# Optimization experiments

Hardware: AMD Instinct MI355X
Metric: run time of the kernel (lower is better)

Reference implementation:

```python
import jax, jax.numpy as jnp
import numpy as np

N_QUBITS = 8
N_QLAYERS = 4
N_HEADS = 4
DIM = 2 ** N_QUBITS  # 256


def layer_norm(x, g, b, eps=1e-5):
    m = x.mean(-1, keepdims=True)
    v = ((x - m) ** 2).mean(-1, keepdims=True)
    return (x - m) / jnp.sqrt(v + eps) * g + b


def rx_mat(theta):
    # theta: scalar or [B]; returns [...,2,2] complex64
    h = theta * 0.5
    c = jnp.cos(h).astype(jnp.complex64)
    s = (jnp.sin(h) * (-1j)).astype(jnp.complex64)
    return jnp.stack([jnp.stack([c, s], -1), jnp.stack([s, c], -1)], -2)


def rz_mat(theta):
    h = (theta * 0.5).astype(jnp.complex64)
    e0 = jnp.exp(-1j * h)
    e1 = jnp.exp(1j * h)
    z = jnp.zeros_like(e0)
    return jnp.stack([jnp.stack([e0, z], -1), jnp.stack([z, e1], -1)], -2)


def apply_1q(state, U, wire, n):
    # state: [B, 2**n]; U: [2,2] (shared) or [B,2,2] (per-sample)
    B = state.shape[0]
    left = 2 ** wire
    right = 2 ** (n - 1 - wire)
    s = state.reshape(B, left, 2, right)
    if U.ndim == 2:
        s = jnp.einsum('jk,blkr->bljr', U, s)
    else:
        s = jnp.einsum('bjk,blkr->bljr', U, s)
    return s.reshape(B, 2 ** n)


def apply_cnot(state, ctrl, n):
    # CNOT with control=ctrl, target=ctrl+1 (adjacent wires)
    B = state.shape[0]
    left = 2 ** ctrl
    right = 2 ** (n - 2 - ctrl)
    s = state.reshape(B, left, 4, right)
    s = s[:, :, jnp.array([0, 1, 3, 2]), :]  # swap |10> and |11>
    return s.reshape(B, 2 ** n)


def quantum_expvals(angles, weights):
    # angles: [B, n_qubits] data-encoding angles; weights: [n_layers, 2, n_qubits]
    # Batched statevector sim of: RX(a_i)RZ(a_i) encoding, then per layer
    # RX(w[l,0,i]) RZ(w[l,1,i]) and a CNOT chain; returns <Z_i> per wire.
    n = N_QUBITS
    B = angles.shape[0]
    state = jnp.zeros((B, 2 ** n), jnp.complex64).at[:, 0].set(1.0)
    for i in range(n):
        state = apply_1q(state, rx_mat(angles[:, i]), i, n)
        state = apply_1q(state, rz_mat(angles[:, i]), i, n)
    for l in range(N_QLAYERS):
        for i in range(n):
            state = apply_1q(state, rx_mat(weights[l, 0, i]), i, n)
            state = apply_1q(state, rz_mat(weights[l, 1, i]), i, n)
        for i in range(n - 1):
            state = apply_cnot(state, i, n)
    probs = jnp.abs(state) ** 2  # [B, 2**n] float32
    zs = []
    for i in range(n):
        p = probs.reshape(B, 2 ** i, 2, 2 ** (n - 1 - i)).sum(axis=(1, 3))
        zs.append(p[:, 0] - p[:, 1])
    return jnp.stack(zs, -1)  # [B, n_qubits]


def mha(x, in_w, in_b, out_w, out_b):
    B, S, d = x.shape
    hd = d // N_HEADS
    qkv = x @ in_w.T + in_b  # [B,S,3d]
    q, k, v = jnp.split(qkv, 3, axis=-1)
    sp = lambda t: t.reshape(B, S, N_HEADS, hd).transpose(0, 2, 1, 3)
    q, k, v = sp(q), sp(k), sp(v)
    scores = jnp.einsum('bhqd,bhkd->bhqk', q, k) / np.sqrt(hd).astype(np.float32)
    attn = jax.nn.softmax(scores, axis=-1)
    o = jnp.einsum('bhqk,bhkd->bhqd', attn, v).transpose(0, 2, 1, 3).reshape(B, S, d)
    return o @ out_w.T + out_b


def _forward(x, attn_in_w, attn_in_b, attn_out_w, attn_out_b,
             ln1_g, ln1_b, ln2_g, ln2_b, ln3_g, ln3_b,
             qin_w, qin_b, qweights, qout_w, qout_b,
             ffn_w1, ffn_b1, ffn_w2, ffn_b2):
    attn_out = mha(x, attn_in_w, attn_in_b, attn_out_w, attn_out_b)
    x = layer_norm(x + attn_out, ln1_g, ln1_b)
    x_norm = layer_norm(x, ln3_g, ln3_b)
    B, S, d = x.shape
    flat = x_norm.reshape(B * S, d)
    angles = flat @ qin_w.T + qin_b  # [B*S, n_qubits]
    z = quantum_expvals(angles, qweights)
    q_out = (z @ qout_w.T + qout_b).reshape(B, S, d)
    x = x + q_out
    h = jax.nn.gelu(x @ ffn_w1.T + ffn_b1, approximate=False)  # torch GELU exact
    ffn_out = h @ ffn_w2.T + ffn_b2  # dropout is identity in eval
    return layer_norm(x + ffn_out, ln2_g, ln2_b)


def setup_inputs() -> dict:
    key = jax.random.key(0)
    ks = jax.random.split(key, 10)
    B, S, d, nq, nl = 32, 512, 512, N_QUBITS, N_QLAYERS
    rn = lambda k, sh, sc=0.02: jax.random.normal(k, sh, jnp.float32) * sc
    return {
        'x': jax.random.normal(ks[0], (B, S, d), jnp.float32),
        'attn_in_w': rn(ks[1], (3 * d, d)),
        'attn_in_b': jnp.zeros((3 * d,), jnp.float32),
        'attn_out_w': rn(ks[2], (d, d)),
        'attn_out_b': jnp.zeros((d,), jnp.float32),
        'ln1_g': jnp.ones((d,), jnp.float32), 'ln1_b': jnp.zeros((d,), jnp.float32),
        'ln2_g': jnp.ones((d,), jnp.float32), 'ln2_b': jnp.zeros((d,), jnp.float32),
        'ln3_g': jnp.ones((d,), jnp.float32), 'ln3_b': jnp.zeros((d,), jnp.float32),
        'qin_w': rn(ks[3], (nq, d), 0.05),
        'qin_b': jnp.zeros((nq,), jnp.float32),
        'qweights': jax.random.uniform(ks[4], (nl, 2, nq), jnp.float32, 0.0, 2.0 * np.pi),
        'qout_w': rn(ks[5], (d, nq), 0.1),
        'qout_b': jnp.zeros((d,), jnp.float32),
        'ffn_w1': rn(ks[6], (4 * d, d)),
        'ffn_b1': jnp.zeros((4 * d,), jnp.float32),
        'ffn_w2': rn(ks[7], (d, 4 * d)),
        'ffn_b2': jnp.zeros((d,), jnp.float32),
    }


def reference(x, attn_in_w, attn_in_b, attn_out_w, attn_out_b,
              ln1_g, ln1_b, ln2_g, ln2_b, ln3_g, ln3_b,
              qin_w, qin_b, qweights, qout_w, qout_b,
              ffn_w1, ffn_b1, ffn_w2, ffn_b2):
    return _forward(x, attn_in_w, attn_in_b, attn_out_w, attn_out_b,
                    ln1_g, ln1_b, ln2_g, ln2_b, ln3_g, ln3_b,
                    qin_w, qin_b, qweights, qout_w, qout_b,
                    ffn_w1, ffn_b1, ffn_w2, ffn_b2)
```

## Files before the change

kernel.cpp:

```cpp
#include <hip/hip_runtime.h>
#include <math.h>


typedef __bf16 bf16;
typedef bf16 bf16x8 __attribute__((ext_vector_type(8)));
typedef bf16 bf16x4 __attribute__((ext_vector_type(4)));
typedef float f32x4 __attribute__((ext_vector_type(4)));

__device__ __forceinline__ void gld16(const void* g, void* l) {
  __builtin_amdgcn_global_load_lds(
      (__attribute__((address_space(1))) void*)(void*)g,
      (__attribute__((address_space(3))) void*)l, 16, 0, 0);
}

__device__ __forceinline__ float waveAllSum(float v) {
#pragma unroll
  for (int m = 1; m < 64; m <<= 1) v += __shfl_xor(v, m, 64);
  return v;
}

__device__ __forceinline__ float fast_gelu(float v) {
  float u = 0.79788456080286536f * v * (1.0f + 0.044715f * v * v);
  return v / (1.0f + __expf(-2.0f * u));
}

__global__ __launch_bounds__(256) void cvt_all(
    const float* __restrict__ x, const float* __restrict__ w1,
    const float* __restrict__ w2, const float* __restrict__ w3,
    const float* __restrict__ w4, bf16* __restrict__ xb,
    bf16* __restrict__ b1, bf16* __restrict__ b2, bf16* __restrict__ b3,
    bf16* __restrict__ b4) {
  int i = blockIdx.x * 256 + threadIdx.x;
  const float* src;
  bf16* dst;
  int off;
  if (i < 2097152) {
    src = x; dst = xb; off = i;
  } else if (i < 2097152 + 196608) {
    src = w1; dst = b1; off = i - 2097152;
  } else if (i < 2097152 + 196608 + 65536) {
    src = w2; dst = b2; off = i - (2097152 + 196608);
  } else if (i < 2097152 + 196608 + 65536 + 262144) {
    src = w3; dst = b3; off = i - (2097152 + 196608 + 65536);
  } else {
    src = w4; dst = b4; off = i - (2097152 + 196608 + 65536 + 262144);
  }
  float4 v = ((const float4*)src)[off];
  bf16x4 o = {(bf16)v.x, (bf16)v.y, (bf16)v.z, (bf16)v.w};
  ((bf16x4*)dst)[off] = o;
}

__global__ __launch_bounds__(256) void make_W(const float* __restrict__ qw,
                                              bf16* __restrict__ Wp) {
  __shared__ float gates[32 * 8];
  int tid = threadIdx.x, lane = tid & 63;
  if (tid < 32) {
    int l = tid >> 3, i = tid & 7;
    float ax = qw[l * 16 + i] * 0.5f;
    float az = qw[l * 16 + 8 + i] * 0.5f;
    float cx, sx, cz, sz;
    sincosf(ax, &sx, &cx);
    sincosf(az, &sz, &cz);
    float* g = gates + tid * 8;
    g[0] = cz * cx;   g[1] = -sz * cx;
    g[2] = -sz * sx;  g[3] = -cz * sx;
    g[4] = sz * sx;   g[5] = -cz * sx;
    g[6] = cz * cx;   g[7] = sz * cx;
  }
  __syncthreads();
  int k = blockIdx.x * 4 + (tid >> 6);

  float sr[4], si[4];
#pragma unroll
  for (int l = 0; l < 4; ++l) {
    sr[l] = (lane * 4 + l == k) ? 1.0f : 0.0f;
    si[l] = 0.0f;
  }

  auto gate = [&](int p, float u00r, float u00i, float u01r, float u01i,
                  float u10r, float u10i, float u11r, float u11i) {
    if (p >= 2) {
      int m = 1 << (p - 2);
      int b = (lane >> (p - 2)) & 1;
      float csr = b ? u11r : u00r;
      float csi = b ? u11i : u00i;
      float cor = b ? u10r : u01r;
      float coi = b ? u10i : u01i;
#pragma unroll
      for (int l = 0; l < 4; ++l) {
        float pr = __shfl_xor(sr[l], m, 64);
        float pi = __shfl_xor(si[l], m, 64);
        float nr = fmaf(csr, sr[l],
                        fmaf(-csi, si[l], fmaf(cor, pr, -coi * pi)));
        float ni = fmaf(csr, si[l],
                        fmaf(csi, sr[l], fmaf(cor, pi, coi * pr)));
        sr[l] = nr;
        si[l] = ni;
      }
    } else {
      float nr[4], ni[4];
#pragma unroll
      for (int l = 0; l < 4; ++l) {
        int b = (l >> p) & 1;
        int pl = l ^ (1 << p);
        float csr = b ? u11r : u00r;
        float csi = b ? u11i : u00i;
        float cor = b ? u10r : u01r;
        float coi = b ? u10i : u01i;
        nr[l] = fmaf(csr, sr[l],
                     fmaf(-csi, si[l], fmaf(cor, sr[pl], -coi * si[pl])));
        ni[l] = fmaf(csr, si[l],
                     fmaf(csi, sr[l], fmaf(cor, si[pl], coi * sr[pl])));
      }
#pragma unroll
      for (int l = 0; l < 4; ++l) {
        sr[l] = nr[l];
        si[l] = ni[l];
      }
    }
  };
  auto docnot = [&](int i) {
    int pc = 7 - i, pt = 6 - i;
    if (pt >= 2) {
      int ctrl = (lane >> (pc - 2)) & 1;
      int m = 1 << (pt - 2);
#pragma unroll
      for (int l = 0; l < 4; ++l) {
        float pr = __shfl_xor(sr[l], m, 64);
        float pi = __shfl_xor(si[l], m, 64);
        if (ctrl) {
          sr[l] = pr;
          si[l] = pi;
        }
      }
    } else if (pt == 1) {
      if (lane & 1) {
        float t;
        t = sr[0]; sr[0] = sr[2]; sr[2] = t;
        t = si[0]; si[0] = si[2]; si[2] = t;
        t = sr[1]; sr[1] = sr[3]; sr[3] = t;
        t = si[1]; si[1] = si[3]; si[3] = t;
      }
    } else {
      float t;
      t = sr[2]; sr[2] = sr[3]; sr[3] = t;
      t = si[2]; si[2] = si[3]; si[3] = t;
    }
  };

  for (int l = 0; l < 4; ++l) {
    for (int i = 0; i < 8; ++i) {
      const float* g = gates + (l * 8 + i) * 8;
      gate(7 - i, g[0], g[1], g[2], g[3], g[4], g[5], g[6], g[7]);
    }
    for (int i = 0; i < 7; ++i) docnot(i);
  }

#pragma unroll
  for (int l = 0; l < 4; ++l) {
    int j = lane * 4 + l;
    Wp[(2 * j) * 512 + k] = (bf16)sr[l];
    Wp[(2 * j) * 512 + 256 + k] = (bf16)(-si[l]);
    Wp[(2 * j + 1) * 512 + k] = (bf16)si[l];
    Wp[(2 * j + 1) * 512 + 256 + k] = (bf16)sr[l];
  }
}

__global__ __launch_bounds__(256) void make_Q(const float* __restrict__ qout_w,
                                              bf16* __restrict__ Q) {
  int t = blockIdx.x * 256 + threadIdx.x;
  int col = t >> 8, k = t & 255;
  float s = 0.f;
#pragma unroll
  for (int w = 0; w < 8; ++w) {
    float sg = ((k >> (7 - w)) & 1) ? -1.0f : 1.0f;
    s = fmaf(qout_w[col * 8 + w], sg, s);
  }
  Q[col * 256 + k] = (bf16)s;
}

__global__ __launch_bounds__(256) void gemm_mfma(
    const bf16* __restrict__ A, const bf16* __restrict__ W,
    const float* __restrict__ bias, const bf16* __restrict__ Xadd,
    bf16* __restrict__ Cb, bf16* __restrict__ qk, bf16* __restrict__ vT,
    bf16* __restrict__ prob, int M, int N, int K, int mode) {
  __shared__ __align__(16) bf16 As[128 * 64];
  __shared__ __align__(16) bf16 Bs[128 * 64];
  int tid = threadIdx.x;
  int lane = tid & 63, w = tid >> 6;
  int wr = w >> 1, wc = w & 1;
  int quad = lane >> 4, lc = lane & 15;
  long m0 = (long)blockIdx.x * 128;
  long n0 = (long)blockIdx.y * 128;
  f32x4 acc[4][4] = {};
  int sl0 = w * 256 + lane;

  const bf16* aSrc[4];
  const bf16* bSrc[4];
  int ldsOff[4];
#pragma unroll
  for (int c = 0; c < 4; ++c) {
    int slot = sl0 + c * 64;
    int row = slot >> 3, g = slot & 7;
    int sc = (g ^ (row & 7)) << 3;
    aSrc[c] = A + (m0 + row) * (long)K + sc;
    bSrc[c] = W + (n0 + row) * (long)K + sc;
    ldsOff[c] = slot << 3;
  }

  for (int k0 = 0; k0 < K; k0 += 64) {
    __syncthreads();
#pragma unroll
    for (int c = 0; c < 4; ++c) {
      gld16(aSrc[c], &As[ldsOff[c]]);
      gld16(bSrc[c], &Bs[ldsOff[c]]);
      aSrc[c] += 64;
      bSrc[c] += 64;
    }
    __syncthreads();
#pragma unroll
    for (int t = 0; t < 2; ++t) {
      bf16x8 af[4], bfr[4];
      int pg = ((t * 4 + quad) ^ (lc & 7)) << 3;
#pragma unroll
      for (int i = 0; i < 4; ++i) {
        af[i] = *(const bf16x8*)&As[(wr * 64 + i * 16 + lc) * 64 + pg];
        bfr[i] = *(const bf16x8*)&Bs[(wc * 64 + i * 16 + lc) * 64 + pg];
      }
#pragma unroll
      for (int i = 0; i < 4; ++i)
#pragma unroll
        for (int j = 0; j < 4; ++j)
          acc[i][j] = __builtin_amdgcn_mfma_f32_16x16x32_bf16(
              af[i], bfr[j], acc[i][j], 0, 0, 0);
    }
  }

#pragma unroll
  for (int i = 0; i < 4; ++i) {
    long grow0 = m0 + wr * 64 + i * 16 + quad * 4;
#pragma unroll
    for (int j = 0; j < 4; ++j) {
      long col = n0 + wc * 64 + j * 16 + lc;
      float bv = (mode == 6) ? 0.f : bias[col];
      float v[4];
#pragma unroll
      for (int r = 0; r < 4; ++r) v[r] = acc[i][j][r] + bv;
      if (mode == 1) {
#pragma unroll
        for (int r = 0; r < 4; ++r)
          Cb[(grow0 + r) * N + col] = (bf16)fast_gelu(v[r]);
      } else if (mode == 4) {
#pragma unroll
        for (int r = 0; r < 4; ++r)
          Cb[(grow0 + r) * N + col] =
              (bf16)(v[r] + (float)Xadd[(grow0 + r) * N + col]);
      } else if (mode == 5) {
#pragma unroll
        for (int r = 0; r < 4; ++r) Cb[(grow0 + r) * N + col] = (bf16)v[r];
      } else if (mode == 6) {
        float pv[4];
#pragma unroll
        for (int r = 0; r < 4; ++r) pv[r] = v[r] * v[r];
#pragma unroll
        for (int r = 0; r < 4; ++r) pv[r] += __shfl_xor(pv[r], 1, 64);
        if (!(lc & 1)) {
          long pc = col >> 1;
#pragma unroll
          for (int r = 0; r < 4; ++r)
            prob[(grow0 + r) * 256 + pc] = (bf16)pv[r];
        }
      } else {
        if (col < 1024) {
#pragma unroll
          for (int r = 0; r < 4; ++r) qk[(grow0 + r) * 1024 + col] = (bf16)v[r];
        } else {
          int hh = (int)((col - 1024) >> 7);
          int dd = (int)((col - 1024) & 127);
          long bidx = grow0 >> 9;
          int s0 = (int)(grow0 & 511);
          bf16x4 pk = {(bf16)v[0], (bf16)v[1], (bf16)v[2], (bf16)v[3]};
          *(bf16x4*)&vT[(((bidx << 2) + hh) * 128 + dd) * 512 + s0] = pk;
        }
      }
    }
  }
}

__global__ __launch_bounds__(256) void attn_mfma(const bf16* __restrict__ qk,
                                                 const bf16* __restrict__ vT,
                                                 bf16* __restrict__ o) {
  __shared__ __align__(16) bf16 Ks[64 * 128];
  __shared__ __align__(16) bf16 Vt[128 * 64];
  __shared__ __align__(16) bf16 Ps[4][64 * 16];
  int tid = threadIdx.x, lane = tid & 63, w = tid >> 6;
  int quad = lane >> 4, lc = lane & 15;
  int bh = blockIdx.x, b = bh >> 2, h = bh & 3;
  int q0 = blockIdx.y * 64 + w * 16;
  const float scale = 0.08838834764831845f;

  bf16x8 qf[4];
  {
    const bf16* qp =
        qk + ((long)(b * 512 + q0 + lc)) * 1024 + h * 128 + quad * 8;
#pragma unroll
    for (int ks = 0; ks < 4; ++ks) qf[ks] = *(const bf16x8*)(qp + ks * 32);
  }
  f32x4 oacc[8] = {};
  float lrun[4] = {0.f, 0.f, 0.f, 0.f};

  const bf16* kbase = qk + (long)b * 512 * 1024 + 512 + h * 128;
  const bf16* vbase = vT + (long)bh * 128 * 512;
  int sl0 = w * 256 + lane;

  const bf16* kSrc[4];
  const bf16* vSrc[4];
  int kOff[4], vOff[4];
#pragma unroll
  for (int c = 0; c < 4; ++c) {
    int slot = sl0 + c * 64;
    {
      int row = slot >> 4, g = slot & 15;
      kSrc[c] = kbase + (long)row * 1024 + ((g ^ (row & 15)) << 3);
      kOff[c] = slot << 3;
    }
    {
      int row = slot >> 3, g = slot & 7;
      vSrc[c] = vbase + (long)row * 512 + ((g ^ (row & 7)) << 3);
      vOff[c] = slot << 3;
    }
  }

  for (int kt = 0; kt < 512; kt += 64) {
    __syncthreads();
#pragma unroll
    for (int c = 0; c < 4; ++c) {
      gld16(kSrc[c], &Ks[kOff[c]]);
      gld16(vSrc[c], &Vt[vOff[c]]);
      kSrc[c] += 64 * 1024;
      vSrc[c] += 64;
    }
    __syncthreads();

    float p[4][4];
#pragma unroll
    for (int c = 0; c < 4; ++c) {
      f32x4 a = {};
#pragma unroll
      for (int ks = 0; ks < 4; ++ks) {
        bf16x8 kf = *(const bf16x8*)&Ks[(c * 16 + lc) * 128 +
                                        (((ks * 4 + quad) ^ lc) << 3)];
        a = __builtin_amdgcn_mfma_f32_16x16x32_bf16(qf[ks], kf, a, 0, 0, 0);
      }
#pragma unroll
      for (int r = 0; r < 4; ++r) p[c][r] = a[r] * scale;
    }

#pragma unroll
    for (int r = 0; r < 4; ++r) {
      float rs = 0.f;
#pragma unroll
      for (int c = 0; c < 4; ++c) {
        float e = __expf(p[c][r]);
        p[c][r] = e;
        rs += e;
      }
#pragma unroll
      for (int m = 1; m < 16; m <<= 1) rs += __shfl_xor(rs, m, 64);
      lrun[r] += rs;
    }

#pragma unroll
    for (int c = 0; c < 4; ++c) {
      bf16x4 pk = {(bf16)p[c][0], (bf16)p[c][1], (bf16)p[c][2], (bf16)p[c][3]};
      *(bf16x4*)&Ps[w][(c * 16 + lc) * 16 + ((quad ^ (lc & 3)) << 2)] = pk;
    }
    bf16x8 pf[2];
#pragma unroll
    for (int kc = 0; kc < 2; ++kc) {
      bf16x8 t;
#pragma unroll
      for (int jj = 0; jj < 8; ++jj) {
        int row = kc * 32 + quad * 8 + jj;
        t[jj] = Ps[w][row * 16 + (((lc >> 2) ^ (row & 3)) << 2) + (lc & 3)];
      }
      pf[kc] = t;
    }
#pragma unroll
    for (int n = 0; n < 8; ++n)
#pragma unroll
      for (int kc = 0; kc < 2; ++kc) {
        bf16x8 vf = *(const bf16x8*)&Vt[(n * 16 + lc) * 64 +
                                        (((kc * 4 + quad) ^ (lc & 7)) << 3)];
        oacc[n] =
            __builtin_amdgcn_mfma_f32_16x16x32_bf16(pf[kc], vf, oacc[n], 0, 0, 0);
      }
  }

  float linv[4];
#pragma unroll
  for (int r = 0; r < 4; ++r) linv[r] = 1.0f / lrun[r];
  bf16* op = o + ((long)(b * 512 + q0 + quad * 4)) * 512 + h * 128 + lc;
#pragma unroll
  for (int n = 0; n < 8; ++n)
#pragma unroll
    for (int r = 0; r < 4; ++r)
      op[(long)r * 512 + n * 16] = (bf16)(oacc[n][r] * linv[r]);
}

__global__ __launch_bounds__(256) void add_ln_bb(
    const bf16* __restrict__ a, const bf16* __restrict__ b,
    const float* __restrict__ g, const float* __restrict__ be,
    float* __restrict__ out) {
  long row = (blockIdx.x * 256 + threadIdx.x) >> 6;
  int lane = threadIdx.x & 63;
  const bf16* ar = a + row * 512;
  const bf16* br = b + row * 512;
  float v[8];
  float s = 0.f;
#pragma unroll
  for (int j = 0; j < 8; ++j) {
    int c = lane + 64 * j;
    v[j] = (float)ar[c] + (float)br[c];
    s += v[j];
  }
  s = waveAllSum(s);
  float mean = s * (1.0f / 512.0f);
  float var = 0.f;
#pragma unroll
  for (int j = 0; j < 8; ++j) {
    float d = v[j] - mean;
    var = fmaf(d, d, var);
  }
  var = waveAllSum(var);
  float rstd = rsqrtf(var * (1.0f / 512.0f) + 1e-5f);
  float* orow = out + row * 512;
#pragma unroll
  for (int j = 0; j < 8; ++j) {
    int c = lane + 64 * j;
    orow[c] = (v[j] - mean) * rstd * g[c] + be[c];
  }
}

__global__ __launch_bounds__(256) void quantum_pre(
    const bf16* __restrict__ xb, const bf16* __restrict__ attnpb,
    const float* __restrict__ g1, const float* __restrict__ b1,
    const float* __restrict__ g3, const float* __restrict__ b3,
    const float* __restrict__ qin_w, const float* __restrict__ qin_b,
    bf16* __restrict__ x1out, bf16* __restrict__ psi) {
  long row = (blockIdx.x * 256 + threadIdx.x) >> 6;
  int lane = threadIdx.x & 63;
  const bf16* xr = xb + row * 512;
  const bf16* ar = attnpb + row * 512;

  float x1v[8];
  {
    float s = 0.f;
#pragma unroll
    for (int j = 0; j < 8; ++j) {
      int c = lane + 64 * j;
      x1v[j] = (float)xr[c] + (float)ar[c];
      s += x1v[j];
    }
    s = waveAllSum(s);
    float mean = s * (1.0f / 512.0f);
    float var = 0.f;
#pragma unroll
    for (int j = 0; j < 8; ++j) {
      float d = x1v[j] - mean;
      var = fmaf(d, d, var);
    }
    var = waveAllSum(var);
    float rstd = rsqrtf(var * (1.0f / 512.0f) + 1e-5f);
#pragma unroll
    for (int j = 0; j < 8; ++j) {
      int c = lane + 64 * j;
      x1v[j] = (x1v[j] - mean) * rstd * g1[c] + b1[c];
    }
  }
  bf16* x1row = x1out + row * 512;
#pragma unroll
  for (int j = 0; j < 8; ++j) x1row[lane + 64 * j] = (bf16)x1v[j];

  float xn[8];
  {
    float s = 0.f;
#pragma unroll
    for (int j = 0; j < 8; ++j) s += x1v[j];
    s = waveAllSum(s);
    float mean = s * (1.0f / 512.0f);
    float var = 0.f;
#pragma unroll
    for (int j = 0; j < 8; ++j) {
      float d = x1v[j] - mean;
      var = fmaf(d, d, var);
    }
    var = waveAllSum(var);
    float rstd = rsqrtf(var * (1.0f / 512.0f) + 1e-5f);
#pragma unroll
    for (int j = 0; j < 8; ++j) {
      int c = lane + 64 * j;
      xn[j] = (x1v[j] - mean) * rstd * g3[c] + b3[c];
    }
  }

  float ang[8];
#pragma unroll
  for (int w = 0; w < 8; ++w) {
    float p = 0.f;
#pragma unroll
    for (int j = 0; j < 8; ++j)
      p = fmaf(xn[j], qin_w[w * 512 + lane + 64 * j], p);
    p = waveAllSum(p);
    ang[w] = p + qin_b[w];
  }

  float v0r[8], v0i[8], v1r[8];
#pragma unroll
  for (int i = 0; i < 8; ++i) {
    float h = ang[i] * 0.5f;
    float c, s;
    sincosf(h, &s, &c);
    v0r[i] = c * c;
    v0i[i] = -c * s;
    v1r[i] = s * s;
  }

  float Pr, Pi;
  {
    int bit0 = (lane >> 5) & 1;
    Pr = bit0 ? v1r[0] : v0r[0];
    Pi = v0i[0];
#pragma unroll
    for (int i = 1; i < 6; ++i) {
      int bit = (lane >> (5 - i)) & 1;
      float br = bit ? v1r[i] : v0r[i];
      float bi = v0i[i];
      float nr = Pr * br - Pi * bi;
      float ni = Pr * bi + Pi * br;
      Pr = nr;
      Pi = ni;
    }
  }

  bf16 rebuf[4], imbuf[4];
#pragma unroll
  for (int l = 0; l < 4; ++l) {
    int b6 = (l >> 1) & 1, b7 = l & 1;
    float br = b6 ? v1r[6] : v0r[6], bi = v0i[6];
    float tr = Pr * br - Pi * bi;
    float ti = Pr * bi + Pi * br;
    float cr = b7 ? v1r[7] : v0r[7], ci = v0i[7];
    float fr = tr * cr - ti * ci;
    float fi = tr * ci + ti * cr;
    rebuf[l] = (bf16)fr;
    imbuf[l] = (bf16)fi;
  }
  bf16* prow = psi + row * 512;
  *(bf16x4*)&prow[lane * 4] = *(bf16x4*)rebuf;
  *(bf16x4*)&prow[256 + lane * 4] = *(bf16x4*)imbuf;
}

extern "C" void kernel_launch(void* const* d_in, const int* in_sizes, int n_in,
                              void* d_out, int out_size, void* d_ws,
                              size_t ws_size, hipStream_t stream) {
  const float* x = (const float*)d_in[0];
  const float* attn_in_w = (const float*)d_in[1];
  const float* attn_in_b = (const float*)d_in[2];
  const float* attn_out_w = (const float*)d_in[3];
  const float* attn_out_b = (const float*)d_in[4];
  const float* ln1_g = (const float*)d_in[5];
  const float* ln1_b = (const float*)d_in[6];
  const float* ln2_g = (const float*)d_in[7];
  const float* ln2_b = (const float*)d_in[8];
  const float* ln3_g = (const float*)d_in[9];
  const float* ln3_b = (const float*)d_in[10];
  const float* qin_w = (const float*)d_in[11];
  const float* qin_b = (const float*)d_in[12];
  const float* qweights = (const float*)d_in[13];
  const float* qout_w = (const float*)d_in[14];
  const float* qout_b = (const float*)d_in[15];
  const float* ffn_w1 = (const float*)d_in[16];
  const float* ffn_b1 = (const float*)d_in[17];
  const float* ffn_w2 = (const float*)d_in[18];
  const float* ffn_b2 = (const float*)d_in[19];

  char* wsB = (char*)d_ws;
  bf16* qkb = (bf16*)(wsB);
  bf16* vtb = (bf16*)(wsB + (32L << 20));
  bf16* ob = (bf16*)(wsB + (48L << 20));
  bf16* hb = (bf16*)(wsB);
  bf16* attnpb = (bf16*)(wsB + (64L << 20));
  bf16* psi = (bf16*)(wsB + (80L << 20));
  bf16* x1b = (bf16*)(wsB + (96L << 20));
  bf16* probb = (bf16*)(wsB + (112L << 20));
  bf16* x2b = (bf16*)(wsB + (120L << 20));
  bf16* f2outb = (bf16*)(wsB + (136L << 20));
  bf16* xb = (bf16*)(wsB + (152L << 20));
  bf16* w_in = (bf16*)(wsB + (168L << 20));
  bf16* w_out = (bf16*)(wsB + (170L << 20));
  bf16* w_f1 = (bf16*)(wsB + (171L << 20));
  bf16* w_f2 = (bf16*)(wsB + (173L << 20));
  bf16* Wp = (bf16*)(wsB + (176L << 20));
  bf16* Qm = (bf16*)(wsB + (177L << 20));

  const int M = 16384;
  float* outp = (float*)d_out;

  cvt_all<<<11264, 256, 0, stream>>>(x, attn_in_w, attn_out_w, ffn_w1, ffn_w2,
                                     xb, w_in, w_out, w_f1, w_f2);
  make_W<<<64, 256, 0, stream>>>(qweights, Wp);
  make_Q<<<512, 256, 0, stream>>>(qout_w, Qm);

  gemm_mfma<<<dim3(M / 128, 12), 256, 0, stream>>>(
      xb, w_in, attn_in_b, nullptr, nullptr, qkb, vtb, nullptr, M, 1536, 512,
      2);
  attn_mfma<<<dim3(128, 8), 256, 0, stream>>>(qkb, vtb, ob);
  gemm_mfma<<<dim3(M / 128, 4), 256, 0, stream>>>(
      ob, w_out, attn_out_b, nullptr, attnpb, nullptr, nullptr, nullptr, M,
      512, 512, 5);
  quantum_pre<<<dim3(M / 4), 256, 0, stream>>>(xb, attnpb, ln1_g, ln1_b,
                                               ln3_g, ln3_b, qin_w, qin_b,
                                               x1b, psi);
  gemm_mfma<<<dim3(M / 128, 4), 256, 0, stream>>>(
      psi, Wp, nullptr, nullptr, nullptr, nullptr, nullptr, probb, M, 512,
      512, 6);
  gemm_mfma<<<dim3(M / 128, 4), 256, 0, stream>>>(
      probb, Qm, qout_b, x1b, x2b, nullptr, nullptr, nullptr, M, 512, 256, 4);
  gemm_mfma<<<dim3(M / 128, 16), 256, 0, stream>>>(
      x2b, w_f1, ffn_b1, nullptr, hb, nullptr, nullptr, nullptr, M, 2048, 512,
      1);
  gemm_mfma<<<dim3(M / 128, 4), 256, 0, stream>>>(
      hb, w_f2, ffn_b2, nullptr, f2outb, nullptr, nullptr, nullptr, M, 512,
      2048, 5);
  add_ln_bb<<<dim3(M / 4), 256, 0, stream>>>(x2b, f2outb, ln2_g, ln2_b, outp);
}
```

Baseline: 431.6 us.

## Prefetch GEMM and attention tiles into registers to overlap loads with MFMA

Replaces the direct global-to-LDS loads in the GEMM and attention kernels with register prefetch. The next K/V or A/B tile is loaded into registers while the current tile's MFMAs run, then written to LDS between barriers. This hides global memory latency behind compute in exchange for extra VGPRs and explicit LDS store instructions, which may lower occupancy.

```diff
diff --git a/kernel.cpp b/kernel.cpp
--- a/kernel.cpp
+++ b/kernel.cpp
@@ -6,12 +6,6 @@
 typedef bf16 bf16x8 __attribute__((ext_vector_type(8)));
 typedef bf16 bf16x4 __attribute__((ext_vector_type(4)));
 typedef float f32x4 __attribute__((ext_vector_type(4)));
-
-__device__ __forceinline__ void gld16(const void* g, void* l) {
-  __builtin_amdgcn_global_load_lds(
-      (__attribute__((address_space(1))) void*)(void*)g,
-      (__attribute__((address_space(3))) void*)l, 16, 0, 0);
-}
 
 __device__ __forceinline__ float waveAllSum(float v) {
 #pragma unroll
@@ -208,16 +202,33 @@
     ldsOff[c] = slot << 3;
   }
 
-  for (int k0 = 0; k0 < K; k0 += 64) {
-    __syncthreads();
-#pragma unroll
-    for (int c = 0; c < 4; ++c) {
-      gld16(aSrc[c], &As[ldsOff[c]]);
-      gld16(bSrc[c], &Bs[ldsOff[c]]);
-      aSrc[c] += 64;
-      bSrc[c] += 64;
-    }
-    __syncthreads();
+  bf16x8 pa[4], pb[4];
+#pragma unroll
+  for (int c = 0; c < 4; ++c) {
+    pa[c] = *(const bf16x8*)aSrc[c];
+    pb[c] = *(const bf16x8*)bSrc[c];
+    aSrc[c] += 64;
+    bSrc[c] += 64;
+  }
+#pragma unroll
+  for (int c = 0; c < 4; ++c) {
+    *(bf16x8*)&As[ldsOff[c]] = pa[c];
+    *(bf16x8*)&Bs[ldsOff[c]] = pb[c];
+  }
+  __syncthreads();
+
+  int iters = K >> 6;
+  for (int it = 0; it < iters; ++it) {
+    bool more = (it + 1 < iters);
+    if (more) {
+#pragma unroll
+      for (int c = 0; c < 4; ++c) {
+        pa[c] = *(const bf16x8*)aSrc[c];
+        pb[c] = *(const bf16x8*)bSrc[c];
+        aSrc[c] += 64;
+        bSrc[c] += 64;
+      }
+    }
 #pragma unroll
     for (int t = 0; t < 2; ++t) {
       bf16x8 af[4], bfr[4];
@@ -234,6 +245,15 @@
           acc[i][j] = __builtin_amdgcn_mfma_f32_16x16x32_bf16(
               af[i], bfr[j], acc[i][j], 0, 0, 0);
     }
+    __syncthreads();
+    if (more) {
+#pragma unroll
+      for (int c = 0; c < 4; ++c) {
+        *(bf16x8*)&As[ldsOff[c]] = pa[c];
+        *(bf16x8*)&Bs[ldsOff[c]] = pb[c];
+      }
+    }
+    __syncthreads();
   }
 
 #pragma unroll
@@ -331,16 +351,32 @@
     }
   }
 
+  bf16x8 pk_[4], pv_[4];
+#pragma unroll
+  for (int c = 0; c < 4; ++c) {
+    pk_[c] = *(const bf16x8*)kSrc[c];
+    pv_[c] = *(const bf16x8*)vSrc[c];
+    kSrc[c] += 64 * 1024;
+    vSrc[c] += 64;
+  }
+#pragma unroll
+  for (int c = 0; c < 4; ++c) {
+    *(bf16x8*)&Ks[kOff[c]] = pk_[c];
+    *(bf16x8*)&Vt[vOff[c]] = pv_[c];
+  }
+  __syncthreads();
+
   for (int kt = 0; kt < 512; kt += 64) {
-    __syncthreads();
-#pragma unroll
-    for (int c = 0; c < 4; ++c) {
-      gld16(kSrc[c], &Ks[kOff[c]]);
-      gld16(vSrc[c], &Vt[vOff[c]]);
-      kSrc[c] += 64 * 1024;
-      vSrc[c] += 64;
-    }
-    __syncthreads();
+    bool more = (kt + 64 < 512);
+    if (more) {
+#pragma unroll
+      for (int c = 0; c < 4; ++c) {
+        pk_[c] = *(const bf16x8*)kSrc[c];
+        pv_[c] = *(const bf16x8*)vSrc[c];
+        kSrc[c] += 64 * 1024;
+        vSrc[c] += 64;
+      }
+    }
 
     float p[4][4];
 #pragma unroll
@@ -395,6 +431,16 @@
         oacc[n] =
             __builtin_amdgcn_mfma_f32_16x16x32_bf16(pf[kc], vf, oacc[n], 0, 0, 0);
       }
+
+    __syncthreads();
+    if (more) {
+#pragma unroll
+      for (int c = 0; c < 4; ++c) {
+        *(bf16x8*)&Ks[kOff[c]] = pk_[c];
+        *(bf16x8*)&Vt[vOff[c]] = pv_[c];
+      }
+    }
+    __syncthreads();
   }
 
   float linv[4];
```

Result: faster. 416.2 us (-3.6%).
